# Performance work log

Measured on AMD Instinct MI355X. Metric: run time of the kernel, lower is better.

## Reference

```python
import jax, jax.numpy as jnp
import numpy as np

B, N, H = 1048576, 6, 32

def setup_inputs() -> dict:
    key = jax.random.key(0)
    k = jax.random.split(key, 6)
    return {
        "x": jax.random.normal(k[0], (B, N), dtype=jnp.float32),
        "A_param": jax.random.normal(k[1], (N, N), dtype=jnp.float32),
        "W1": jax.random.normal(k[2], (H, 1), dtype=jnp.float32) * (1.0),  # Linear(1,H) weight
        "b1": jax.random.normal(k[3], (H,), dtype=jnp.float32) * 0.1,
        "W2": jax.random.normal(k[4], (1, H), dtype=jnp.float32) * (1.0 / np.sqrt(H)),
        "b2": jax.random.normal(k[5], (1,), dtype=jnp.float32) * 0.1,
    }

def reference(x, A_param, W1, b1, W2, b2):
    # A = softmax over rows of learned adjacency  [N, N]
    A = jax.nn.softmax(A_param, axis=-1)
    # fc1: per-node scalar -> hidden  [B, N, H]
    h = x[..., None] * W1[:, 0] + b1
    # graph mixing: A @ h  [B, N, H]
    h = jnp.einsum('mn,bnh->bmh', A, h)
    h = jax.nn.relu(h)
    # fc2: hidden -> scalar, squeeze  [B, N]
    h = jnp.einsum('bnh,h->bn', h, W2[0]) + b2[0]
    return x + h
```

## Files before the change

### kernel.cpp

```cpp
#include <hip/hip_runtime.h>
#include <math.h>


typedef float f32x2 __attribute__((ext_vector_type(2)));
typedef float f32x4 __attribute__((ext_vector_type(4)));

#define NN 6
#define HH 32
#define NB 512
#define YMIN  (-8.0f)
#define YSPAN (16.0f)
#define INVH  ((float)NB / YSPAN)
#define OFFS  (-YMIN * INVH)
#define BINW  (YSPAN / (float)NB)

__device__ __forceinline__ f32x2 mk2(float a, float b) {
    f32x2 r; r.x = a; r.y = b; return r;
}

__device__ __forceinline__ f32x2 pk_fma(f32x2 a, f32x2 b, f32x2 c) {
#if __has_builtin(__builtin_elementwise_fma)
    return __builtin_elementwise_fma(a, b, c);
#else
    f32x2 r; r.x = fmaf(a.x, b.x, c.x); r.y = fmaf(a.y, b.y, c.y); return r;
#endif
}

__device__ __forceinline__ void eval_pair(
    f32x4 v0, f32x4 v1, f32x4 v2,
    const float* __restrict__ sA,
    const f32x2* __restrict__ sTab,
    f32x4& o0, f32x4& o1, f32x4& o2)
{
    f32x2 xx[NN];
    xx[0] = mk2(v0.x, v1.z);
    xx[1] = mk2(v0.y, v1.w);
    xx[2] = mk2(v0.z, v2.x);
    xx[3] = mk2(v0.w, v2.y);
    xx[4] = mk2(v1.x, v2.z);
    xx[5] = mk2(v1.y, v2.w);

    f32x2 yy[NN];
#pragma unroll
    for (int m = 0; m < NN; ++m) {
        f32x2 a = mk2(0.f, 0.f);
#pragma unroll
        for (int n = 0; n < NN; ++n) {
            float c = sA[m * NN + n];
            a = pk_fma(mk2(c, c), xx[n], a);
        }
        yy[m] = a;
    }

    f32x2 rr[NN];
#pragma unroll
    for (int m = 0; m < NN; ++m) {
#pragma unroll
        for (int half = 0; half < 2; ++half) {
            float yv = half ? yy[m].y : yy[m].x;
            float fi = fmaf(yv, INVH, OFFS);
            fi = fminf(fmaxf(fi, 0.0f), (float)(NB - 1));
            int k = (int)fi;
            f32x2 ab = sTab[k];
            float r = fmaf(ab.y, yv, ab.x);
            if (half) rr[m].y = r; else rr[m].x = r;
        }
    }

    o0.x = v0.x + rr[0].x;
    o0.y = v0.y + rr[1].x;
    o0.z = v0.z + rr[2].x;
    o0.w = v0.w + rr[3].x;
    o1.x = v1.x + rr[4].x;
    o1.y = v1.y + rr[5].x;
    o1.z = v1.z + rr[0].y;
    o1.w = v1.w + rr[1].y;
    o2.x = v2.x + rr[2].y;
    o2.y = v2.y + rr[3].y;
    o2.z = v2.z + rr[4].y;
    o2.w = v2.w + rr[5].y;
}

__global__ __launch_bounds__(256) void graph_block_fused(
    const float* __restrict__ x,
    const float* __restrict__ Ap,
    const float* __restrict__ W1p,
    const float* __restrict__ b1p,
    const float* __restrict__ W2p,
    const float* __restrict__ b2p,
    float* __restrict__ out,
    int nPairs)
{
    __shared__ float sA[NN * NN];
    __shared__ float sW1[HH], sB1[HH], sW2[HH];
    __shared__ float sB2;
    __shared__ float sEdge[NB + 1];
    __shared__ __align__(16) f32x2 sTab[NB];

    const int tid = threadIdx.x;
    const int tA = blockIdx.x * 512 + tid;
    const int tB = tA + 256;
    const bool vA = (tA < nPairs);
    const bool vB = (tB < nPairs);

    f32x4 a0, a1, a2, b0, b1v, b2v;
    if (vA) {
        const f32x4* __restrict__ p = (const f32x4*)(x + (size_t)tA * 12);
        a0 = p[0]; a1 = p[1]; a2 = p[2];
    }
    if (vB) {
        const f32x4* __restrict__ p = (const f32x4*)(x + (size_t)tB * 12);
        b0 = p[0]; b1v = p[1]; b2v = p[2];
    }

    if (tid < HH) {
        sW1[tid] = W1p[tid];
        sB1[tid] = b1p[tid];
        sW2[tid] = W2p[tid];
    }
    if (tid == HH) sB2 = b2p[0];
    if (tid >= 64 && tid < 64 + NN) {
        int m = tid - 64;
        float r[NN];
        float mx = -INFINITY;
#pragma unroll
        for (int n = 0; n < NN; ++n) {
            r[n] = Ap[m * NN + n];
            mx = fmaxf(mx, r[n]);
        }
        float s = 0.f;
#pragma unroll
        for (int n = 0; n < NN; ++n) {
            r[n] = expf(r[n] - mx);
            s += r[n];
        }
        float inv = 1.f / s;
#pragma unroll
        for (int n = 0; n < NN; ++n) sA[m * NN + n] = r[n] * inv;
    }
    __syncthreads();

    {
        float bb2 = sB2;
        float e0 = YMIN + (float)tid * BINW;
        float e1 = e0 + 256.0f * BINW;
        float f0 = bb2, f1 = bb2;
#pragma unroll
        for (int h = 0; h < HH; ++h) {
            float w1 = sW1[h];
            float bv = sB1[h];
            float w2 = sW2[h];
            f0 = fmaf(fmaxf(fmaf(w1, e0, bv), 0.f), w2, f0);
            f1 = fmaf(fmaxf(fmaf(w1, e1, bv), 0.f), w2, f1);
        }
        sEdge[tid] = f0;
        sEdge[tid + 256] = f1;
        if (tid == 0) {
            float f2 = bb2;
#pragma unroll
            for (int h = 0; h < HH; ++h)
                f2 = fmaf(fmaxf(fmaf(sW1[h], YMIN + YSPAN, sB1[h]), 0.f), sW2[h], f2);
            sEdge[NB] = f2;
        }
    }
    __syncthreads();

#pragma unroll
    for (int i = 0; i < 2; ++i) {
        int k = tid + i * 256;
        float fa = sEdge[k];
        float fb = sEdge[k + 1];
        float beta = (fb - fa) * INVH;
        float ek = YMIN + (float)k * BINW;
        sTab[k] = mk2(fmaf(-beta, ek, fa), beta);
    }
    __syncthreads();

    if (vA) {
        f32x4 o0, o1, o2;
        eval_pair(a0, a1, a2, sA, sTab, o0, o1, o2);
        f32x4* __restrict__ ov = (f32x4*)(out + (size_t)tA * 12);
        ov[0] = o0; ov[1] = o1; ov[2] = o2;
    }
    if (vB) {
        f32x4 o0, o1, o2;
        eval_pair(b0, b1v, b2v, sA, sTab, o0, o1, o2);
        f32x4* __restrict__ ov = (f32x4*)(out + (size_t)tB * 12);
        ov[0] = o0; ov[1] = o1; ov[2] = o2;
    }
}

extern "C" void kernel_launch(void* const* d_in, const int* in_sizes, int n_in,
                              void* d_out, int out_size, void* d_ws, size_t ws_size,
                              hipStream_t stream) {
    const float* x  = (const float*)d_in[0];
    const float* Ap = (const float*)d_in[1];
    const float* W1 = (const float*)d_in[2];
    const float* b1 = (const float*)d_in[3];
    const float* W2 = (const float*)d_in[4];
    const float* b2 = (const float*)d_in[5];
    float* out = (float*)d_out;

    int nPairs = in_sizes[0] / 12;
    int grid = (nPairs + 511) / 512;
    graph_block_fused<<<grid, 256, 0, stream>>>(x, Ap, W1, b1, W2, b2, out, nPairs);
}
```

Measured before the change: 17.67 us.

## Stage input and output through LDS for fully coalesced float4 global accesses

Before, each thread loaded and stored three consecutive float4s, a 48-byte stride across lanes. Now the block loads x with consecutive float4s per lane, stages them in shared memory, computes from the per-thread view, writes the results back to shared memory, then stores coalesced. It also adds a launch-bounds occupancy hint of 4 blocks. In exchange it uses about 24KB of extra LDS per block plus one more barrier, and the LDS reads at a 3-float4 thread stride may cause bank conflicts.

```diff
diff --git a/kernel.cpp b/kernel.cpp
--- a/kernel.cpp
+++ b/kernel.cpp
@@ -13,6 +13,8 @@
 #define INVH  ((float)NB / YSPAN)
 #define OFFS  (-YMIN * INVH)
 #define BINW  (YSPAN / (float)NB)
+#define CPB   2
+#define F4C   768
 
 __device__ __forceinline__ f32x2 mk2(float a, float b) {
     f32x2 r; r.x = a; r.y = b; return r;
@@ -81,7 +83,7 @@
     o2.w = v2.w + rr[5].y;
 }
 
-__global__ __launch_bounds__(256) void graph_block_fused(
+__global__ __launch_bounds__(256, 4) void graph_block_fused(
     const float* __restrict__ x,
     const float* __restrict__ Ap,
     const float* __restrict__ W1p,
@@ -96,22 +98,20 @@
     __shared__ float sB2;
     __shared__ float sEdge[NB + 1];
     __shared__ __align__(16) f32x2 sTab[NB];
+    __shared__ __align__(16) float sX[CPB][F4C * 4];
 
     const int tid = threadIdx.x;
-    const int tA = blockIdx.x * 512 + tid;
-    const int tB = tA + 256;
-    const bool vA = (tA < nPairs);
-    const bool vB = (tB < nPairs);
-
-    f32x4 a0, a1, a2, b0, b1v, b2v;
-    if (vA) {
-        const f32x4* __restrict__ p = (const f32x4*)(x + (size_t)tA * 12);
-        a0 = p[0]; a1 = p[1]; a2 = p[2];
-    }
-    if (vB) {
-        const f32x4* __restrict__ p = (const f32x4*)(x + (size_t)tB * 12);
-        b0 = p[0]; b1v = p[1]; b2v = p[2];
-    }
+    const int nF4 = nPairs * 3;
+    const int blockF4 = blockIdx.x * (CPB * F4C);
+
+    f32x4 st[CPB][3];
+#pragma unroll
+    for (int c = 0; c < CPB; ++c)
+#pragma unroll
+        for (int j = 0; j < 3; ++j) {
+            int f4 = blockF4 + c * F4C + j * 256 + tid;
+            if (f4 < nF4) st[c][j] = ((const f32x4*)x)[f4];
+        }
 
     if (tid < HH) {
         sW1[tid] = W1p[tid];
@@ -147,9 +147,7 @@
         float f0 = bb2, f1 = bb2;
 #pragma unroll
         for (int h = 0; h < HH; ++h) {
-            float w1 = sW1[h];
-            float bv = sB1[h];
-            float w2 = sW2[h];
+            float w1 = sW1[h], bv = sB1[h], w2 = sW2[h];
             f0 = fmaf(fmaxf(fmaf(w1, e0, bv), 0.f), w2, f0);
             f1 = fmaf(fmaxf(fmaf(w1, e1, bv), 0.f), w2, f1);
         }
@@ -163,6 +161,11 @@
             sEdge[NB] = f2;
         }
     }
+#pragma unroll
+    for (int c = 0; c < CPB; ++c)
+#pragma unroll
+        for (int j = 0; j < 3; ++j)
+            ((f32x4*)sX[c])[j * 256 + tid] = st[c][j];
     __syncthreads();
 
 #pragma unroll
@@ -176,18 +179,23 @@
     }
     __syncthreads();
 
-    if (vA) {
+#pragma unroll
+    for (int c = 0; c < CPB; ++c) {
+        f32x4* ps = (f32x4*)sX[c] + tid * 3;
+        f32x4 v0 = ps[0], v1 = ps[1], v2 = ps[2];
         f32x4 o0, o1, o2;
-        eval_pair(a0, a1, a2, sA, sTab, o0, o1, o2);
-        f32x4* __restrict__ ov = (f32x4*)(out + (size_t)tA * 12);
-        ov[0] = o0; ov[1] = o1; ov[2] = o2;
-    }
-    if (vB) {
-        f32x4 o0, o1, o2;
-        eval_pair(b0, b1v, b2v, sA, sTab, o0, o1, o2);
-        f32x4* __restrict__ ov = (f32x4*)(out + (size_t)tB * 12);
-        ov[0] = o0; ov[1] = o1; ov[2] = o2;
-    }
+        eval_pair(v0, v1, v2, sA, sTab, o0, o1, o2);
+        ps[0] = o0; ps[1] = o1; ps[2] = o2;
+    }
+    __syncthreads();
+
+#pragma unroll
+    for (int c = 0; c < CPB; ++c)
+#pragma unroll
+        for (int j = 0; j < 3; ++j) {
+            int f4 = blockF4 + c * F4C + j * 256 + tid;
+            if (f4 < nF4) ((f32x4*)out)[f4] = ((const f32x4*)sX[c])[j * 256 + tid];
+        }
 }
 
 extern "C" void kernel_launch(void* const* d_in, const int* in_sizes, int n_in,
```

After: 15.86 us. -10.2%, faster.
